# Performance work log

Hardware: AMD Instinct MI355X
Metric: run time of the kernel (lower is better)

Reference implementation:

```python
import jax, jax.numpy as jnp
import numpy as np

B, S, E = 2, 2048, 2048
H, D = 16, 128  # num_attention_heads, head_dim = hidden_size // num_heads


def rotate_half(x):
    x1 = x[..., : x.shape[-1] // 2]
    x2 = x[..., x.shape[-1] // 2 :]
    return jnp.concatenate((-x2, x1), axis=-1)


def setup_inputs() -> dict:
    key = jax.random.key(0)
    ks = jax.random.split(key, 7)
    return {
        "hidden_states": jax.random.normal(ks[0], (B, S, E), dtype=jnp.float32),
        "cos": jax.random.uniform(ks[1], (1, 1, S, D), dtype=jnp.float32),
        "sin": jax.random.uniform(ks[2], (1, 1, S, D), dtype=jnp.float32),
        "wq": jax.random.normal(ks[3], (E, H * D), dtype=jnp.float32) / np.sqrt(E),
        "wk": jax.random.normal(ks[4], (E, H * D), dtype=jnp.float32) / np.sqrt(E),
        "wv": jax.random.normal(ks[5], (E, H * D), dtype=jnp.float32) / np.sqrt(E),
        "wo": jax.random.normal(ks[6], (H * D, E), dtype=jnp.float32) / np.sqrt(H * D),
    }


def reference(hidden_states, cos, sin, wq, wk, wv, wo):
    # QKV projections (no bias, per attention_bias=False)
    q = (hidden_states @ wq).reshape(B, S, H, D).transpose(0, 2, 1, 3)  # bhsd
    k = (hidden_states @ wk).reshape(B, S, H, D).transpose(0, 2, 1, 3)
    v = (hidden_states @ wv).reshape(B, S, H, D).transpose(0, 2, 1, 3)
    # RoPE (applied after the head transpose, as in the original)
    q = q * cos + rotate_half(q) * sin
    k = k * cos + rotate_half(k) * sin
    # NOTE: original forward never applies self.scaling and uses no causal mask.
    scores = jnp.einsum("bhqd,bhkd->bhqk", q, k)
    attn = jax.nn.softmax(scores.astype(jnp.float32), axis=-1)
    out = jnp.einsum("bhqk,bhkd->bhqd", attn, v)
    out = out.transpose(0, 2, 1, 3).reshape(B, S, H * D)
    return out @ wo
```

## Files before the change

kernel.cpp:

```cpp
#include <hip/hip_runtime.h>
#include <stdint.h>

typedef _Float16 f16;
typedef _Float16 half8 __attribute__((ext_vector_type(8)));
typedef _Float16 half4 __attribute__((ext_vector_type(4)));
typedef __fp16 fp16x2 __attribute__((ext_vector_type(2)));
typedef float f32x4 __attribute__((ext_vector_type(4)));
typedef float f32x16 __attribute__((ext_vector_type(16)));
typedef uint32_t u32x4 __attribute__((ext_vector_type(4)));

static constexpr int Bsz = 2, S = 2048, E = 2048, H = 16, D = 128;
static constexpr int M = Bsz * S;
static constexpr int N_QKV = 3 * H * D;
static constexpr int HD = H * D;

__device__ __forceinline__ void gload_lds16(const void* gp, void* lp) {
  __builtin_amdgcn_global_load_lds(
      (const __attribute__((address_space(1))) uint32_t*)(uintptr_t)gp,
      (__attribute__((address_space(3))) uint32_t*)(uint32_t)(uintptr_t)lp,
      16, 0, 0);
}

__device__ __forceinline__ uint32_t pkrtz(float a, float b) {
  fp16x2 r = __builtin_amdgcn_cvt_pkrtz(a, b);
  return __builtin_bit_cast(uint32_t, r);
}

__global__ void cast_f32_f16(const float* __restrict__ in, f16* __restrict__ out) {
  size_t i = (size_t)(blockIdx.x * 256 + threadIdx.x) * 8;
  float4 a = *(const float4*)&in[i];
  float4 b = *(const float4*)&in[i + 4];
  half8 h;
  h[0] = (f16)a.x; h[1] = (f16)a.y; h[2] = (f16)a.z; h[3] = (f16)a.w;
  h[4] = (f16)b.x; h[5] = (f16)b.y; h[6] = (f16)b.z; h[7] = (f16)b.w;
  *(half8*)&out[i] = h;
}

__global__ void transpose_cast(const float* __restrict__ wq, const float* __restrict__ wk,
                               const float* __restrict__ wv, const float* __restrict__ wo,
                               f16* __restrict__ wt, f16* __restrict__ wot) {
  __shared__ float tile[32][33];
  int z = blockIdx.z;
  const float* src = (z == 0) ? wq : (z == 1) ? wk : (z == 2) ? wv : wo;
  f16* dst = (z == 3) ? wot : wt + (size_t)z * E * HD;
  int bx = blockIdx.x * 32, by = blockIdx.y * 32;
  int tx = threadIdx.x, ty = threadIdx.y;
#pragma unroll
  for (int r = 0; r < 4; ++r)
    tile[ty + r * 8][tx] = src[(size_t)(by + ty + r * 8) * 2048 + bx + tx];
  __syncthreads();
#pragma unroll
  for (int r = 0; r < 4; ++r)
    dst[(size_t)(bx + ty + r * 8) * 2048 + by + tx] = (f16)tile[tx][ty + r * 8];
}

template <typename OutT>
__global__ __launch_bounds__(256, 2) void gemm_bt(const f16* __restrict__ A,
                                                  const f16* __restrict__ Bt,
                                                  OutT* __restrict__ C,
                                                  int Mm, int Nn, int Kk) {
  __shared__ f16 As[128 * 32];
  __shared__ f16 Bs[128 * 32];
  const int t = threadIdx.x, l = t & 63;
  const int wm = (t >> 7) & 1, wn = (t >> 6) & 1;
  const int bm = blockIdx.x, bn = blockIdx.y;
  const int lr = l & 15, g = l >> 4;
  const int srow = t >> 2;
  const int schunk = t & 3;
  const int scol = ((schunk ^ (srow & 3)) * 8);
  const size_t abase = (size_t)(bm * 128 + srow) * Kk;
  const size_t bbase = (size_t)(bn * 128 + srow) * Kk;
  f32x4 acc[4][4] = {};
  for (int k0 = 0; k0 < Kk; k0 += 32) {
    __syncthreads();
    gload_lds16(&A[abase + k0 + scol], &As[t * 8]);
    gload_lds16(&A[abase + (size_t)64 * Kk + k0 + scol], &As[2048 + t * 8]);
    gload_lds16(&Bt[bbase + k0 + scol], &Bs[t * 8]);
    gload_lds16(&Bt[bbase + (size_t)64 * Kk + k0 + scol], &Bs[2048 + t * 8]);
    __syncthreads();
    half8 af[4], bf[4];
#pragma unroll
    for (int i = 0; i < 4; ++i) {
      int ra = wm * 64 + i * 16 + lr;
      int rb = wn * 64 + i * 16 + lr;
      af[i] = *(const half8*)&As[ra * 32 + ((g ^ (ra & 3)) * 8)];
      bf[i] = *(const half8*)&Bs[rb * 32 + ((g ^ (rb & 3)) * 8)];
    }
#pragma unroll
    for (int i = 0; i < 4; ++i)
#pragma unroll
      for (int j = 0; j < 4; ++j)
        acc[i][j] = __builtin_amdgcn_mfma_f32_16x16x32_f16(af[i], bf[j], acc[i][j], 0, 0, 0);
  }
#pragma unroll
  for (int i = 0; i < 4; ++i)
#pragma unroll
    for (int j = 0; j < 4; ++j) {
      int row = bm * 128 + wm * 64 + i * 16 + g * 4;
      int col = bn * 128 + wn * 64 + j * 16 + lr;
#pragma unroll
      for (int r = 0; r < 4; ++r)
        C[(size_t)(row + r) * Nn + col] = (OutT)acc[i][j][r];
    }
}

__global__ void rope_split(const f16* __restrict__ qkv, const float* __restrict__ cosb,
                           const float* __restrict__ sinb, f16* __restrict__ Q,
                           f16* __restrict__ Ko) {
  int idx = blockIdx.x * 256 + threadIdx.x;
  int d4 = idx & 15;
  int h = (idx >> 4) & 15;
  int s = (idx >> 8) & 2047;
  int b = idx >> 19;
  int d = d4 * 4;
  size_t mrow = (size_t)(b * S + s) * N_QKV;
  const f16* q = &qkv[mrow + h * D];
  const f16* k = &qkv[mrow + HD + h * D];
  size_t ob = ((size_t)(b * H + h) * S + s) * D;
  float4 c1 = *(const float4*)&cosb[s * D + d];
  float4 c2 = *(const float4*)&cosb[s * D + 64 + d];
  float4 s1 = *(const float4*)&sinb[s * D + d];
  float4 s2 = *(const float4*)&sinb[s * D + 64 + d];
  float c1a[4] = {c1.x, c1.y, c1.z, c1.w}, c2a[4] = {c2.x, c2.y, c2.z, c2.w};
  float s1a[4] = {s1.x, s1.y, s1.z, s1.w}, s2a[4] = {s2.x, s2.y, s2.z, s2.w};
  half4 qlo = *(const half4*)&q[d], qhi = *(const half4*)&q[d + 64];
  half4 klo = *(const half4*)&k[d], khi = *(const half4*)&k[d + 64];
  half4 oql, oqh, okl, okh;
#pragma unroll
  for (int j = 0; j < 4; ++j) {
    float ql = (float)qlo[j], qh = (float)qhi[j];
    float kl = (float)klo[j], kh = (float)khi[j];
    oql[j] = (f16)(ql * c1a[j] - qh * s1a[j]);
    oqh[j] = (f16)(qh * c2a[j] + ql * s2a[j]);
    okl[j] = (f16)(kl * c1a[j] - kh * s1a[j]);
    okh[j] = (f16)(kh * c2a[j] + kl * s2a[j]);
  }
  *(half4*)&Q[ob + d] = oql;  *(half4*)&Q[ob + d + 64] = oqh;
  *(half4*)&Ko[ob + d] = okl; *(half4*)&Ko[ob + d + 64] = okh;
}

__global__ void transpose_v(const f16* __restrict__ qkv, f16* __restrict__ VtG) {
  __shared__ f16 tl[64][136];
  int bid = blockIdx.x;
  int bh = bid >> 5, st = bid & 31;
  int b = bh >> 4, h = bh & 15;
  int t = threadIdx.x;
  int s0 = st * 64;
#pragma unroll
  for (int rnd = 0; rnd < 4; ++rnd) {
    int row = rnd * 16 + (t >> 4);
    int ch = t & 15;
    half8 v = *(const half8*)&qkv[(size_t)(b * S + s0 + row) * N_QKV + 2 * HD + h * D + ch * 8];
    *(half8*)&tl[row][ch * 8] = v;
  }
  __syncthreads();
#pragma unroll
  for (int rnd = 0; rnd < 4; ++rnd) {
    int d = rnd * 32 + (t >> 3);
    int ch = t & 7;
    half8 v;
#pragma unroll
    for (int j = 0; j < 8; ++j) v[j] = tl[ch * 8 + j][d];
    *(half8*)&VtG[((size_t)bh * D + d) * S + s0 + ch * 8] = v;
  }
}

__device__ __forceinline__ void stage_kv(const f16* __restrict__ Kg, const f16* __restrict__ Vg,
                                         f16* KsB, f16* VsB, int t, int kv) {
#pragma unroll
  for (int rnd = 0; rnd < 4; ++rnd) {
    int row = rnd * 16 + (t >> 4);
    int c = t & 15;
    gload_lds16(&Kg[(size_t)(kv + row) * D + ((c ^ (row & 7)) * 8)], &KsB[rnd * 2048 + t * 8]);
  }
#pragma unroll
  for (int rnd = 0; rnd < 4; ++rnd) {
    int row = rnd * 32 + (t >> 3);
    int c = t & 7;
    gload_lds16(&Vg[(size_t)row * S + kv + ((c ^ (row & 7)) * 8)], &VsB[rnd * 2048 + t * 8]);
  }
}

__global__ __launch_bounds__(256, 2) void flash_attn2(const f16* __restrict__ Q,
                                                      const f16* __restrict__ K,
                                                      const f16* __restrict__ Vt,
                                                      f16* __restrict__ O) {
  __shared__ f16 lds[2][16384];
  const int t = threadIdx.x, l = t & 63, w = t >> 6;
  const int c = l & 31, hi = l >> 5;
  int bid = blockIdx.x;
  bid = (bid & 7) * 64 + (bid >> 3);
  const int bh = bid >> 4, qt = bid & 15;
  const size_t baseQ = (size_t)bh * S * D;
  const f16* Kg = K + baseQ;
  const f16* Vg = Vt + (size_t)bh * D * S;
  const int q0 = qt * 128 + w * 32;
  half8 qf[8];
#pragma unroll
  for (int dc = 0; dc < 8; ++dc)
    qf[dc] = *(const half8*)&Q[baseQ + (size_t)(q0 + c) * D + dc * 16 + hi * 8];
  f32x16 o[4] = {};
  float m = -3.0e38f, ssum = 0.f;

  stage_kv(Kg, Vg, &lds[0][0], &lds[0][8192], t, 0);
  __syncthreads();

  for (int it = 0; it < S / 64; ++it) {
    const int cur = it & 1;
    const f16* KsB = &lds[cur][0];
    const f16* VsB = &lds[cur][8192];
    if (it + 1 < S / 64) stage_kv(Kg, Vg, &lds[cur ^ 1][0], &lds[cur ^ 1][8192], t, (it + 1) * 64);

    f32x16 s0 = {}, s1 = {};
    __builtin_amdgcn_s_setprio(1);
#pragma unroll
    for (int dc = 0; dc < 8; ++dc) {
      const int r0 = c, r1 = 32 + c;
      half8 kf0 = *(const half8*)&KsB[r0 * 128 + (((2 * dc + hi) ^ (r0 & 7)) * 8)];
      half8 kf1 = *(const half8*)&KsB[r1 * 128 + (((2 * dc + hi) ^ (r1 & 7)) * 8)];
      s0 = __builtin_amdgcn_mfma_f32_32x32x16_f16(kf0, qf[dc], s0, 0, 0, 0);
      s1 = __builtin_amdgcn_mfma_f32_32x32x16_f16(kf1, qf[dc], s1, 0, 0, 0);
    }
    __builtin_amdgcn_s_setprio(0);

    float tm = s0[0];
#pragma unroll
    for (int r = 1; r < 16; ++r) tm = fmaxf(tm, s0[r]);
#pragma unroll
    for (int r = 0; r < 16; ++r) tm = fmaxf(tm, s1[r]);
    tm = fmaxf(tm, __shfl_xor(tm, 32));
    float mn = fmaxf(m, tm);
    float corr = __expf(m - mn);
    m = mn;
    float ts = 0.f;
#pragma unroll
    for (int r = 0; r < 16; ++r) { s0[r] = __expf(s0[r] - mn); ts += s0[r]; }
#pragma unroll
    for (int r = 0; r < 16; ++r) { s1[r] = __expf(s1[r] - mn); ts += s1[r]; }
    ts += __shfl_xor(ts, 32);
    ssum = ssum * corr + ts;
#pragma unroll
    for (int dt = 0; dt < 4; ++dt)
#pragma unroll
      for (int r = 0; r < 16; ++r) o[dt][r] *= corr;

    half8 pf[4];
#pragma unroll
    for (int ks = 0; ks < 4; ++ks) {
      const int B0 = 2 * (ks & 1), B1 = B0 + 1;
      uint32_t X0, X1, Y0, Y1;
      if (ks < 2) {
        X0 = pkrtz(s0[4 * B0 + 0], s0[4 * B0 + 1]);
        X1 = pkrtz(s0[4 * B0 + 2], s0[4 * B0 + 3]);
        Y0 = pkrtz(s0[4 * B1 + 0], s0[4 * B1 + 1]);
        Y1 = pkrtz(s0[4 * B1 + 2], s0[4 * B1 + 3]);
      } else {
        X0 = pkrtz(s1[4 * B0 + 0], s1[4 * B0 + 1]);
        X1 = pkrtz(s1[4 * B0 + 2], s1[4 * B0 + 3]);
        Y0 = pkrtz(s1[4 * B1 + 0], s1[4 * B1 + 1]);
        Y1 = pkrtz(s1[4 * B1 + 2], s1[4 * B1 + 3]);
      }
      asm volatile("v_permlane32_swap_b32 %0, %1" : "+v"(X0), "+v"(Y0));
      asm volatile("v_permlane32_swap_b32 %0, %1" : "+v"(X1), "+v"(Y1));
      u32x4 pw; pw[0] = X0; pw[1] = X1; pw[2] = Y0; pw[3] = Y1;
      pf[ks] = __builtin_bit_cast(half8, pw);
    }

    __builtin_amdgcn_s_setprio(1);
#pragma unroll
    for (int dt = 0; dt < 4; ++dt) {
      const int row = dt * 32 + c;
#pragma unroll
      for (int ks = 0; ks < 4; ++ks) {
        half8 vf = *(const half8*)&VsB[row * 64 + (((2 * ks + hi) ^ (row & 7)) * 8)];
        o[dt] = __builtin_amdgcn_mfma_f32_32x32x16_f16(vf, pf[ks], o[dt], 0, 0, 0);
      }
    }
    __builtin_amdgcn_s_setprio(0);
    __syncthreads();
  }

  const float inv = 1.f / ssum;
  const int b = bh >> 4, h = bh & 15;
  const size_t orow = ((size_t)(b * S + q0 + c)) * HD + h * D;
#pragma unroll
  for (int dt = 0; dt < 4; ++dt)
#pragma unroll
    for (int b2 = 0; b2 < 4; ++b2) {
      half4 h4;
#pragma unroll
      for (int a = 0; a < 4; ++a) h4[a] = (f16)(o[dt][4 * b2 + a] * inv);
      *(half4*)&O[orow + dt * 32 + 8 * b2 + 4 * hi] = h4;
    }
}

extern "C" void kernel_launch(void* const* d_in, const int* in_sizes, int n_in,
                              void* d_out, int out_size, void* d_ws, size_t ws_size,
                              hipStream_t stream) {
  (void)in_sizes; (void)n_in; (void)out_size; (void)ws_size;
  const float* hs = (const float*)d_in[0];
  const float* cosb = (const float*)d_in[1];
  const float* sinb = (const float*)d_in[2];
  const float* wq = (const float*)d_in[3];
  const float* wk = (const float*)d_in[4];
  const float* wv = (const float*)d_in[5];
  const float* wo = (const float*)d_in[6];
  float* out = (float*)d_out;
  char* ws = (char*)d_ws;
  f16* hs16 = (f16*)(ws);
  f16* attn = (f16*)(ws);
  f16* wt   = (f16*)(ws + (16u << 20));
  f16* wot  = (f16*)(ws + (40u << 20));
  f16* qkv  = (f16*)(ws + (48u << 20));
  f16* Qb   = (f16*)(ws + (96u << 20));
  f16* Kb   = (f16*)(ws + (112u << 20));
  f16* VtG  = (f16*)(ws + (128u << 20));

  cast_f32_f16<<<dim3(4096), dim3(256), 0, stream>>>(hs, hs16);
  transpose_cast<<<dim3(64, 64, 4), dim3(32, 8), 0, stream>>>(wq, wk, wv, wo, wt, wot);
  gemm_bt<f16><<<dim3(32, 48), dim3(256), 0, stream>>>(hs16, wt, qkv, M, N_QKV, E);
  rope_split<<<dim3(4096), dim3(256), 0, stream>>>(qkv, cosb, sinb, Qb, Kb);
  transpose_v<<<dim3(1024), dim3(256), 0, stream>>>(qkv, VtG);
  flash_attn2<<<dim3(512), dim3(256), 0, stream>>>(Qb, Kb, VtG, attn);
  gemm_bt<float><<<dim3(32, 16), dim3(256), 0, stream>>>(attn, wot, out, M, E, HD);
}
```

Baseline: 308.4 us.

## Replace GEMM with 256x256-tile double-buffered 8-wave pipelined kernel

```diff
diff --git a/kernel.cpp b/kernel.cpp
--- a/kernel.cpp
+++ b/kernel.cpp
@@ -55,53 +55,108 @@
 }
 
 template <typename OutT>
-__global__ __launch_bounds__(256, 2) void gemm_bt(const f16* __restrict__ A,
-                                                  const f16* __restrict__ Bt,
-                                                  OutT* __restrict__ C,
-                                                  int Mm, int Nn, int Kk) {
-  __shared__ f16 As[128 * 32];
-  __shared__ f16 Bs[128 * 32];
-  const int t = threadIdx.x, l = t & 63;
-  const int wm = (t >> 7) & 1, wn = (t >> 6) & 1;
-  const int bm = blockIdx.x, bn = blockIdx.y;
+__global__ __launch_bounds__(512, 2) void gemm8p(const f16* __restrict__ A,
+                                                 const f16* __restrict__ Bt,
+                                                 OutT* __restrict__ C,
+                                                 int Nn, int Kk, int nbn) {
+  __shared__ f16 lds[65536];
+  const int t = threadIdx.x, l = t & 63, wv = t >> 6;
+  const int wm = wv >> 2, wn = wv & 3;
   const int lr = l & 15, g = l >> 4;
+  const int nwg = gridDim.x;
+  const int bid = blockIdx.x;
+  const int wg = (bid & 7) * (nwg >> 3) + (bid >> 3);
+  const int bm = wg / nbn, bn = wg % nbn;
   const int srow = t >> 2;
-  const int schunk = t & 3;
-  const int scol = ((schunk ^ (srow & 3)) * 8);
-  const size_t abase = (size_t)(bm * 128 + srow) * Kk;
-  const size_t bbase = (size_t)(bn * 128 + srow) * Kk;
-  f32x4 acc[4][4] = {};
-  for (int k0 = 0; k0 < Kk; k0 += 32) {
-    __syncthreads();
-    gload_lds16(&A[abase + k0 + scol], &As[t * 8]);
-    gload_lds16(&A[abase + (size_t)64 * Kk + k0 + scol], &As[2048 + t * 8]);
-    gload_lds16(&Bt[bbase + k0 + scol], &Bs[t * 8]);
-    gload_lds16(&Bt[bbase + (size_t)64 * Kk + k0 + scol], &Bs[2048 + t * 8]);
-    __syncthreads();
-    half8 af[4], bf[4];
-#pragma unroll
-    for (int i = 0; i < 4; ++i) {
-      int ra = wm * 64 + i * 16 + lr;
-      int rb = wn * 64 + i * 16 + lr;
-      af[i] = *(const half8*)&As[ra * 32 + ((g ^ (ra & 3)) * 8)];
-      bf[i] = *(const half8*)&Bs[rb * 32 + ((g ^ (rb & 3)) * 8)];
-    }
-#pragma unroll
-    for (int i = 0; i < 4; ++i)
-#pragma unroll
-      for (int j = 0; j < 4; ++j)
-        acc[i][j] = __builtin_amdgcn_mfma_f32_16x16x32_f16(af[i], bf[j], acc[i][j], 0, 0, 0);
-  }
-#pragma unroll
-  for (int i = 0; i < 4; ++i)
-#pragma unroll
-    for (int j = 0; j < 4; ++j) {
-      int row = bm * 128 + wm * 64 + i * 16 + g * 4;
-      int col = bn * 128 + wn * 64 + j * 16 + lr;
+  const int scol = ((t & 3) ^ (srow & 3)) * 8;
+  const f16* Ab = A + (size_t)(bm * 256 + srow) * Kk + scol;
+  const f16* Bb = Bt + (size_t)(bn * 256 + srow) * Kk + scol;
+  const int NT = Kk >> 6;
+
+#define SEC_A(b, kh) ((b) * 32768 + (kh) * 8192)
+#define SEC_B(b, kh) ((b) * 32768 + 16384 + (kh) * 8192)
+#define STAGE(base, kcol, sec)                             \
+  do {                                                     \
+    const f16* sp_ = (base) + (kcol);                      \
+    gload_lds16(sp_, &lds[(sec) + t * 8]);                 \
+    gload_lds16(sp_ + (size_t)128 * Kk, &lds[(sec) + 4096 + t * 8]); \
+  } while (0)
+#define LDA(kh_, mh_)                                                          \
+  _Pragma("unroll") for (int i = 0; i < 4; ++i) {                              \
+    int ra = wm * 128 + ((mh_)*4 + i) * 16 + lr;                               \
+    a[i] = *(const half8*)&lds[SEC_A(cb, kh_) + ra * 32 + ((g ^ (ra & 3)) * 8)]; \
+  }
+#define LDB(kh_)                                                               \
+  _Pragma("unroll") for (int j = 0; j < 4; ++j) {                              \
+    int rb = wn * 64 + j * 16 + lr;                                            \
+    b[j] = *(const half8*)&lds[SEC_B(cb, kh_) + rb * 32 + ((g ^ (rb & 3)) * 8)]; \
+  }
+#define MFMA16(mh_)                                                            \
+  __builtin_amdgcn_s_setprio(1);                                               \
+  _Pragma("unroll") for (int i = 0; i < 4; ++i)                                \
+  _Pragma("unroll") for (int j = 0; j < 4; ++j)                                \
+      acc[(mh_)*4 + i][j] =                                                    \
+          __builtin_amdgcn_mfma_f32_16x16x32_f16(a[i], b[j], acc[(mh_)*4 + i][j], 0, 0, 0); \
+  __builtin_amdgcn_s_setprio(0);
+#define BAR() __builtin_amdgcn_s_barrier()
+#define VMCNT6() asm volatile("s_waitcnt vmcnt(6)" ::: "memory")
+
+  f32x4 acc[8][4] = {};
+  STAGE(Ab, 0, SEC_A(0, 0));
+  STAGE(Bb, 0, SEC_B(0, 0));
+  STAGE(Ab, 32, SEC_A(0, 1));
+  STAGE(Bb, 32, SEC_B(0, 1));
+  if (NT > 1) {
+    STAGE(Ab, 64, SEC_A(1, 0));
+    STAGE(Bb, 64, SEC_B(1, 0));
+  }
+  asm volatile("s_waitcnt vmcnt(8)" ::: "memory");
+  BAR();
+
+  for (int kt = 0; kt < NT; ++kt) {
+    const int cb = kt & 1;
+    half8 a[4], b[4];
+    LDB(0); LDA(0, 0);
+    if (kt + 1 < NT) STAGE(Ab, (kt + 1) * 64 + 32, SEC_A(cb ^ 1, 1));
+    BAR();
+    MFMA16(0);
+    BAR();
+    LDA(0, 1);
+    if (kt + 1 < NT) STAGE(Bb, (kt + 1) * 64 + 32, SEC_B(cb ^ 1, 1));
+    VMCNT6();
+    BAR();
+    MFMA16(1);
+    BAR();
+    LDB(1); LDA(1, 0);
+    if (kt + 2 < NT) STAGE(Ab, (kt + 2) * 64, SEC_A(cb, 0));
+    BAR();
+    MFMA16(0);
+    BAR();
+    LDA(1, 1);
+    if (kt + 2 < NT) STAGE(Bb, (kt + 2) * 64, SEC_B(cb, 0));
+    VMCNT6();
+    BAR();
+    MFMA16(1);
+    BAR();
+  }
+
+  const int crow = bm * 256 + wm * 128 + g * 4;
+  const int ccol = bn * 256 + wn * 64 + lr;
+#pragma unroll
+  for (int m = 0; m < 8; ++m)
+#pragma unroll
+    for (int n = 0; n < 4; ++n)
 #pragma unroll
       for (int r = 0; r < 4; ++r)
-        C[(size_t)(row + r) * Nn + col] = (OutT)acc[i][j][r];
-    }
+        C[(size_t)(crow + m * 16 + r) * Nn + ccol + n * 16] = (OutT)acc[m][n][r];
+#undef SEC_A
+#undef SEC_B
+#undef STAGE
+#undef LDA
+#undef LDB
+#undef MFMA16
+#undef BAR
+#undef VMCNT6
 }
 
 __global__ void rope_split(const f16* __restrict__ qkv, const float* __restrict__ cosb,
@@ -318,9 +373,9 @@
 
   cast_f32_f16<<<dim3(4096), dim3(256), 0, stream>>>(hs, hs16);
   transpose_cast<<<dim3(64, 64, 4), dim3(32, 8), 0, stream>>>(wq, wk, wv, wo, wt, wot);
-  gemm_bt<f16><<<dim3(32, 48), dim3(256), 0, stream>>>(hs16, wt, qkv, M, N_QKV, E);
+  gemm8p<f16><<<dim3(16 * 24), dim3(512), 0, stream>>>(hs16, wt, qkv, N_QKV, E, 24);
   rope_split<<<dim3(4096), dim3(256), 0, stream>>>(qkv, cosb, sinb, Qb, Kb);
   transpose_v<<<dim3(1024), dim3(256), 0, stream>>>(qkv, VtG);
   flash_attn2<<<dim3(512), dim3(256), 0, stream>>>(Qb, Kb, VtG, attn);
-  gemm_bt<float><<<dim3(32, 16), dim3(256), 0, stream>>>(attn, wot, out, M, E, HD);
-}
+  gemm8p<float><<<dim3(16 * 8), dim3(512), 0, stream>>>(attn, wot, out, E, HD, 8);
+}
```

New measurement: 329.8 us. +6.9%, slower.
